# Kernel tuning notes

Hardware: AMD Instinct MI355X
Metric: run time of the kernel (lower is better)

The kernel has to match this reference:

```python
import jax, jax.numpy as jnp
import numpy as np

N_ANCHORS = 10647
N_CLASSES = 80
N_OUT = 5 + N_CLASSES
N_GT = 2048
POS_IOU = 0.7
NEG_IOU = 0.3
N_SAMPLE = 256
POS_RATIO = 0.5


def _cxcy_to_corners(b):
    return jnp.concatenate([b[:, :2] - b[:, 2:4] / 2, b[:, :2] + b[:, 2:4] / 2], axis=-1)


def _iou(a, b):
    # a: [N,4] corner boxes, b: [M,4] corner boxes -> [N,M]
    lt = jnp.maximum(a[:, None, :2], b[None, :, :2])
    rb = jnp.minimum(a[:, None, 2:], b[None, :, 2:])
    wh = jnp.clip(rb - lt, 0.0)
    inter = wh[..., 0] * wh[..., 1]
    area_a = (a[:, 2] - a[:, 0]) * (a[:, 3] - a[:, 1])
    area_b = (b[:, 2] - b[:, 0]) * (b[:, 3] - b[:, 1])
    return inter / (area_a[:, None] + area_b[None, :] - inter)


def _bce_logits(x, t):
    # numerically stable BCEWithLogits, elementwise
    return jnp.maximum(x, 0.0) - x * t + jnp.log1p(jnp.exp(-jnp.abs(x)))


def _demote_first(labels, value, excess):
    # demote the first `excess` anchors (in index order) whose label == value to -1,
    # mirroring torch's nonzero()[randperm(excess)] which always hits the first
    # `excess` entries of the nonzero list
    m = labels == value
    cum = jnp.cumsum(m.astype(jnp.int32))
    return jnp.where(m & (cum <= excess), -1.0, labels)


def _generate_targets(priors, gt_boxes, gt_labels):
    ious = _iou(_cxcy_to_corners(priors[:, :4]), _cxcy_to_corners(gt_boxes))  # [N, M]
    gt_max_index = jnp.argmax(ious, axis=0)       # [M] best anchor per gt
    anchor_max_ious = jnp.max(ious, axis=1)       # [N]
    anchor_max_index = jnp.argmax(ious, axis=1)   # [N]
    labels = jnp.full((N_ANCHORS,), -1.0, dtype=ious.dtype)
    labels = labels.at[gt_max_index].set(1.0)
    labels = jnp.where(anchor_max_ious >= POS_IOU, 1.0, labels)
    labels = jnp.where(anchor_max_ious < NEG_IOU, 0.0, labels)
    n_pos_quota = int(POS_RATIO * N_SAMPLE)
    n_pos_actual = jnp.sum(labels == 1.0)
    labels = _demote_first(labels, 1.0, jnp.maximum(n_pos_actual - n_pos_quota, 0))
    n_neg_req = N_SAMPLE - jnp.sum(labels == 1.0)
    n_neg_actual = jnp.sum(labels == 0.0)
    labels = _demote_first(labels, 0.0, jnp.maximum(n_neg_actual - n_neg_req, 0))
    anchor_gt_box = gt_boxes[anchor_max_index]    # [N,4] matched gt box per anchor
    anchor_cls = gt_labels[anchor_max_index] + 5  # [N] one-hot class column per anchor
    targets = jnp.zeros((N_ANCHORS, N_OUT), dtype=gt_boxes.dtype)
    targets = targets.at[:, :4].set(anchor_gt_box)
    targets = targets.at[:, 4].set(labels)
    targets = targets.at[jnp.arange(N_ANCHORS), anchor_cls].set(1.0)
    return targets


def _forward(predictions, gt_boxes, gt_labels, priors):
    targets = _generate_targets(priors, gt_boxes, gt_labels)
    pred = predictions[0]                          # [N, N_OUT]
    labels = targets[:, 4]
    pos = (labels == 1.0).astype(pred.dtype)
    neg = (labels == 0.0).astype(pred.dtype)
    n_pos = jnp.maximum(jnp.sum(pos), 1.0)
    n_neg = jnp.maximum(jnp.sum(neg), 1.0)
    # masked-mean MSE over x,y,w,h on positive anchors
    diff2 = (pred[:, :4] - targets[:, :4]) ** 2
    loss_box = jnp.sum(pos[:, None] * diff2, axis=0) / n_pos
    loss_conf_obj = jnp.sum(pos * _bce_logits(pred[:, 4], targets[:, 4])) / n_pos
    loss_conf_nonobj = jnp.sum(neg * _bce_logits(pred[:, 4], targets[:, 4])) / n_neg
    loss_class = jnp.sum(pos[:, None] * _bce_logits(pred[:, 5:], targets[:, 5:])) / (n_pos * N_CLASSES)
    total_loss = jnp.sum(loss_box) + loss_conf_obj + loss_conf_nonobj + loss_class
    return pred, total_loss


def setup_inputs() -> dict:
    key = jax.random.key(0)
    k1, k2, k3, k4 = jax.random.split(key, 4)
    predictions = jax.random.normal(k1, (1, N_ANCHORS, N_OUT), dtype=jnp.float32)
    gt_boxes = jax.random.uniform(k2, (N_GT, 4), dtype=jnp.float32, minval=0.05, maxval=0.95)
    gt_labels = jax.random.randint(k3, (N_GT,), 0, N_CLASSES)
    priors = jax.random.uniform(k4, (N_ANCHORS, N_OUT), dtype=jnp.float32, minval=0.05, maxval=0.95)
    return {"predictions": predictions, "gt_boxes": gt_boxes, "gt_labels": gt_labels, "priors": priors}


def reference(predictions, gt_boxes, gt_labels, priors):
    return _forward(predictions, gt_boxes, gt_labels, priors)
```

## Files before the change

kernel.cpp:

```cpp
#include <hip/hip_runtime.h>
#include <math.h>

#define N_ANCH 10647
#define N_GT   2048
#define N_OUTC 85
#define PRED_ELEMS (N_ANCH * N_OUTC)
#define PRED_V4    (PRED_ELEMS / 4)
#define N_CHUNK    42

#define ABX 21
#define ABY 32
#define NBLK_A (ABX * ABY)
#define GBX 4
#define GBY 167
#define NBLK_G (GBX * GBY)
#define NBLK_IOU (NBLK_A + NBLK_G)
#define CPY_PER_BLK ((PRED_V4 + NBLK_IOU - 1) / NBLK_IOU)

struct WS {
    unsigned long long akey[N_ANCH];
    unsigned long long gkey[N_GT];
    float acc[3];
    float pad_;
    int lab[N_ANCH];
    int cnt_p[N_CHUNK], cnt_n[N_CHUNK];
};
#define MEMSET_BYTES (N_ANCH * 8 + N_GT * 8 + 16)

__device__ __forceinline__ float bce(float x, float t) {
    return fmaxf(x, 0.0f) - x * t + log1pf(expf(-fabsf(x)));
}

__device__ __forceinline__ unsigned long long packkey(float iou, int idx) {
    return ((unsigned long long)__float_as_uint(iou) << 32) |
           (unsigned)(~(unsigned)idx);
}

__global__ __launch_bounds__(256) void k_iou(const float* __restrict__ pred,
                                             const float* __restrict__ gtb,
                                             const float* __restrict__ priors,
                                             float* __restrict__ out,
                                             WS* __restrict__ ws) {
    int b = blockIdx.x, t = threadIdx.x;
    if (t < CPY_PER_BLK) {
        int idx = b * CPY_PER_BLK + t;
        if (idx < PRED_V4)
            ((float4*)out)[idx] = ((const float4*)pred)[idx];
    }
    if (b == 0 && t == 0) {
        out[PRED_ELEMS - 3] = pred[PRED_ELEMS - 3];
        out[PRED_ELEMS - 2] = pred[PRED_ELEMS - 2];
        out[PRED_ELEMS - 1] = pred[PRED_ELEMS - 1];
    }

    __shared__ float4 sc[64];
    __shared__ float  sa[64];

    if (b < NBLK_A) {
        int bx = b % ABX, by = b / ABX;
        int jbase = by * 64;
        if (t < 64) {
            float4 v = ((const float4*)gtb)[jbase + t];
            float4 c = make_float4(v.x - v.z*0.5f, v.y - v.w*0.5f,
                                   v.x + v.z*0.5f, v.y + v.w*0.5f);
            sc[t] = c;
            sa[t] = (c.z - c.x) * (c.w - c.y);
        }
        int i0 = bx * 512 + t, i1 = i0 + 256;
        bool v0 = (i0 < N_ANCH), v1 = (i1 < N_ANCH);
        float4 a0 = make_float4(0.f,0.f,0.f,0.f), a1 = a0;
        float aa0 = 0.f, aa1 = 0.f;
        if (v0) {
            float cx = priors[i0*N_OUTC+0], cy = priors[i0*N_OUTC+1];
            float w  = priors[i0*N_OUTC+2], h  = priors[i0*N_OUTC+3];
            a0 = make_float4(cx - w*0.5f, cy - h*0.5f, cx + w*0.5f, cy + h*0.5f);
            aa0 = (a0.z - a0.x) * (a0.w - a0.y);
        }
        if (v1) {
            float cx = priors[i1*N_OUTC+0], cy = priors[i1*N_OUTC+1];
            float w  = priors[i1*N_OUTC+2], h  = priors[i1*N_OUTC+3];
            a1 = make_float4(cx - w*0.5f, cy - h*0.5f, cx + w*0.5f, cy + h*0.5f);
            aa1 = (a1.z - a1.x) * (a1.w - a1.y);
        }
        __syncthreads();
        float I0 = -1.f, S0 = 1.f, I1 = -1.f, S1 = 1.f;
        int bj0 = 0, bj1 = 0;
#pragma unroll 4
        for (int jj = 0; jj < 64; ++jj) {
            float4 g = sc[jj]; float ga = sa[jj];
            float lx = fmaxf(a0.x, g.x), ly = fmaxf(a0.y, g.y);
            float rx = fminf(a0.z, g.z), ry = fminf(a0.w, g.w);
            float In = fmaxf(rx - lx, 0.f) * fmaxf(ry - ly, 0.f);
            float Sn = aa0 + ga;
            bool c = In * S0 > I0 * Sn;
            I0 = c ? In : I0; S0 = c ? Sn : S0; bj0 = c ? jj : bj0;
            lx = fmaxf(a1.x, g.x); ly = fmaxf(a1.y, g.y);
            rx = fminf(a1.z, g.z); ry = fminf(a1.w, g.w);
            In = fmaxf(rx - lx, 0.f) * fmaxf(ry - ly, 0.f);
            Sn = aa1 + ga;
            c = In * S1 > I1 * Sn;
            I1 = c ? In : I1; S1 = c ? Sn : S1; bj1 = c ? jj : bj1;
        }
        if (v0) atomicMax(&ws->akey[i0], packkey(I0 / (S0 - I0), jbase + bj0));
        if (v1) atomicMax(&ws->akey[i1], packkey(I1 / (S1 - I1), jbase + bj1));
    } else {
        int b2 = b - NBLK_A;
        int bx = b2 % GBX, by = b2 / GBX;
        int ibase = by * 64;
        if (t < 64) {
            int i = ibase + t;
            float4 c = make_float4(0.f, 0.f, 0.f, 0.f);
            float ar = 0.f;
            if (i < N_ANCH) {
                float cx = priors[i*N_OUTC+0], cy = priors[i*N_OUTC+1];
                float w  = priors[i*N_OUTC+2], h  = priors[i*N_OUTC+3];
                c = make_float4(cx - w*0.5f, cy - h*0.5f, cx + w*0.5f, cy + h*0.5f);
                ar = (c.z - c.x) * (c.w - c.y);
            }
            sc[t] = c; sa[t] = ar;
        }
        int j0 = bx * 512 + t, j1 = j0 + 256;
        float4 v = ((const float4*)gtb)[j0];
        float4 g0 = make_float4(v.x - v.z*0.5f, v.y - v.w*0.5f,
                                v.x + v.z*0.5f, v.y + v.w*0.5f);
        float ga0 = (g0.z - g0.x) * (g0.w - g0.y);
        v = ((const float4*)gtb)[j1];
        float4 g1 = make_float4(v.x - v.z*0.5f, v.y - v.w*0.5f,
                                v.x + v.z*0.5f, v.y + v.w*0.5f);
        float ga1 = (g1.z - g1.x) * (g1.w - g1.y);
        __syncthreads();
        float I0 = -1.f, S0 = 1.f, I1 = -1.f, S1 = 1.f;
        int bi0 = 0, bi1 = 0;
#pragma unroll 4
        for (int ii = 0; ii < 64; ++ii) {
            float4 a = sc[ii]; float aa = sa[ii];
            float lx = fmaxf(a.x, g0.x), ly = fmaxf(a.y, g0.y);
            float rx = fminf(a.z, g0.z), ry = fminf(a.w, g0.w);
            float In = fmaxf(rx - lx, 0.f) * fmaxf(ry - ly, 0.f);
            float Sn = aa + ga0;
            bool c = In * S0 > I0 * Sn;
            I0 = c ? In : I0; S0 = c ? Sn : S0; bi0 = c ? ii : bi0;
            lx = fmaxf(a.x, g1.x); ly = fmaxf(a.y, g1.y);
            rx = fminf(a.z, g1.z); ry = fminf(a.w, g1.w);
            In = fmaxf(rx - lx, 0.f) * fmaxf(ry - ly, 0.f);
            Sn = aa + ga1;
            c = In * S1 > I1 * Sn;
            I1 = c ? In : I1; S1 = c ? Sn : S1; bi1 = c ? ii : bi1;
        }
        atomicMax(&ws->gkey[j0], packkey(I0 / (S0 - I0), ibase + bi0));
        atomicMax(&ws->gkey[j1], packkey(I1 / (S1 - I1), ibase + bi1));
    }
}

__global__ __launch_bounds__(256) void k_label(WS* __restrict__ ws) {
    __shared__ int flg[256];
    __shared__ int wp[4], wn[4];
    int b = blockIdx.x, t = threadIdx.x, base = b * 256;
    int lane = t & 63, wid = t >> 6;
    flg[t] = 0;
    __syncthreads();
    for (int j = t; j < N_GT; j += 256) {
        int ai = (int)(~(unsigned)(ws->gkey[j]));
        int rel = ai - base;
        if ((unsigned)rel < 256u) flg[rel] = 1;
    }
    __syncthreads();
    int i = base + t;
    int lab = -2;
    if (i < N_ANCH) {
        float amax = __uint_as_float((unsigned)(ws->akey[i] >> 32));
        lab = (amax < 0.3f) ? 0 : ((amax >= 0.7f || flg[t]) ? 1 : -1);
        ws->lab[i] = lab;
    }
    unsigned long long b1 = __ballot(lab == 1), b0 = __ballot(lab == 0);
    if (lane == 0) { wp[wid] = __popcll(b1); wn[wid] = __popcll(b0); }
    __syncthreads();
    if (t == 0) {
        ws->cnt_p[b] = wp[0] + wp[1] + wp[2] + wp[3];
        ws->cnt_n[b] = wn[0] + wn[1] + wn[2] + wn[3];
    }
}

__global__ __launch_bounds__(256) void k_closs(const float* __restrict__ pred,
                                               const float* __restrict__ gtb,
                                               const int* __restrict__ gtl,
                                               WS* __restrict__ ws) {
    __shared__ int wps[4], wns[4];
    __shared__ int    sPosI[256];
    __shared__ float4 sPosBox[256];
    __shared__ int    sPosCls[256];
    __shared__ int    sNegI[256];
    __shared__ float  red[12];
    int b = blockIdx.x, t = threadIdx.x, lane = t & 63, wid = t >> 6;

    int npa = 0, nna = 0, pb = 0, nb = 0;
#pragma unroll
    for (int c = 0; c < N_CHUNK; ++c) {
        int cp = ws->cnt_p[c], cn = ws->cnt_n[c];
        if (c < b) { pb += cp; nb += cn; }
        npa += cp; nna += cn;
    }
    int excess_pos = (npa > 128) ? (npa - 128) : 0;
    int n_pos_f = npa - excess_pos;
    int n_neg_req = 256 - n_pos_f;
    int excess_neg = (nna > n_neg_req) ? (nna - n_neg_req) : 0;

    int i = b * 256 + t;
    int lab = (i < N_ANCH) ? ws->lab[i] : -2;
    bool f1 = (lab == 1), f0 = (lab == 0);
    unsigned long long b1 = __ballot(f1), b0v = __ballot(f0);
    unsigned long long pm = (2ull << lane) - 1ull;
    int r1 = __popcll(b1 & pm), r0 = __popcll(b0v & pm);
    if (lane == 0) { wps[wid] = __popcll(b1); wns[wid] = __popcll(b0v); }
    __syncthreads();
    int p1 = 0, p0 = 0, cpB = 0, cnB = 0;
    for (int w = 0; w < 4; ++w) {
        int v1 = wps[w], v0 = wns[w];
        cpB += v1; cnB += v0;
        if (w < wid) { p1 += v1; p0 += v0; }
    }
    int thp = excess_pos - pb; thp = (thp < 0) ? 0 : thp;
    int thn = excess_neg - nb; thn = (thn < 0) ? 0 : thn;
    if (f1) {
        int L = p1 + r1;
        if (L > thp) {
            int slot = L - thp - 1;
            sPosI[slot] = i;
            unsigned am = ~(unsigned)(ws->akey[i]);
            sPosBox[slot] = ((const float4*)gtb)[am];
            sPosCls[slot] = gtl[am] + 5;
        }
    }
    if (f0) {
        int L = p0 + r0;
        if (L > thn) sNegI[L - thn - 1] = i;
    }
    __syncthreads();
    int nP = cpB - thp; nP = (nP < 0) ? 0 : nP;
    int nN = cnB - thn; nN = (nN < 0) ? 0 : nN;

    float acc_a = 0.f, acc_c = 0.f, acc_n = 0.f;
    int nT = nP * N_OUTC;
    for (int u = t; u < nT; u += 256) {
        int pi = u / N_OUTC, col = u - pi * N_OUTC;
        float p = pred[sPosI[pi] * N_OUTC + col];
        if (col < 4) {
            float d = p - ((const float*)&sPosBox[pi])[col];
            acc_a += d * d;
        } else if (col == 4) {
            acc_a += bce(p, 1.0f);
        } else {
            acc_c += bce(p, (col == sPosCls[pi]) ? 1.0f : 0.0f);
        }
    }
    for (int u = t; u < nN; u += 256)
        acc_n += bce(pred[sNegI[u] * N_OUTC + 4], 0.0f);

    for (int o = 32; o; o >>= 1) {
        acc_a += __shfl_down(acc_a, o);
        acc_c += __shfl_down(acc_c, o);
        acc_n += __shfl_down(acc_n, o);
    }
    if (lane == 0) { red[wid] = acc_a; red[4 + wid] = acc_c; red[8 + wid] = acc_n; }
    __syncthreads();
    if (t == 0) {
        float A  = red[0] + red[1] + red[2]  + red[3];
        float C  = red[4] + red[5] + red[6]  + red[7];
        float Nn = red[8] + red[9] + red[10] + red[11];
        if (A  != 0.f) atomicAdd(&ws->acc[0], A);
        if (C  != 0.f) atomicAdd(&ws->acc[1], C);
        if (Nn != 0.f) atomicAdd(&ws->acc[2], Nn);
    }
}

__global__ __launch_bounds__(64) void k_final(WS* __restrict__ ws,
                                              float* __restrict__ out) {
    int t = threadIdx.x;
    int cp = (t < N_CHUNK) ? ws->cnt_p[t] : 0;
    int cn = (t < N_CHUNK) ? ws->cnt_n[t] : 0;
    for (int o = 32; o; o >>= 1) { cp += __shfl_down(cp, o); cn += __shfl_down(cn, o); }
    if (t == 0) {
        int npa = cp, nna = cn;
        int excess_pos = (npa > 128) ? (npa - 128) : 0;
        int n_pos_f = npa - excess_pos;
        int n_neg_req = 256 - n_pos_f;
        int excess_neg = (nna > n_neg_req) ? (nna - n_neg_req) : 0;
        int n_neg_f = nna - excess_neg;
        float np = fmaxf((float)n_pos_f, 1.0f);
        float nn = fmaxf((float)n_neg_f, 1.0f);
        out[PRED_ELEMS] = ws->acc[0] / np + ws->acc[2] / nn + ws->acc[1] / (np * 80.0f);
    }
}

extern "C" void kernel_launch(void* const* d_in, const int* in_sizes, int n_in,
                              void* d_out, int out_size, void* d_ws, size_t ws_size,
                              hipStream_t stream) {
    const float* pred   = (const float*)d_in[0];
    const float* gtb    = (const float*)d_in[1];
    const int*   gtl    = (const int*)d_in[2];
    const float* priors = (const float*)d_in[3];
    float* out = (float*)d_out;
    WS* ws = (WS*)d_ws;

    hipMemsetAsync(d_ws, 0, MEMSET_BYTES, stream);
    k_iou<<<dim3(NBLK_IOU), 256, 0, stream>>>(pred, gtb, priors, out, ws);
    k_label<<<dim3(N_CHUNK), 256, 0, stream>>>(ws);
    k_closs<<<dim3(N_CHUNK), 256, 0, stream>>>(pred, gtb, gtl, ws);
    k_final<<<1, 64, 0, stream>>>(ws, out);
}
```

Measured before the change: 69.55 us.

## Fuse label, loss and final kernels into one tail kernel

Merges k_label, k_closs and k_final into a single k_tail kernel. Each block rebuilds the gt-best-anchor flags as a shared bitmap and recomputes labels and counts for all anchors redundantly, which removes the per-chunk count exchange through global memory. Each block then scales its partial losses by the final counts and atomically adds them straight into the output scalar, which k_iou zeroes first. Two kernel launches and their dependency gaps are removed, at the cost of every block scanning all anchor keys and gt keys and of float atomic accumulation order varying between runs.

```diff
diff --git a/kernel.cpp b/kernel.cpp
--- a/kernel.cpp
+++ b/kernel.cpp
@@ -7,6 +7,7 @@
 #define PRED_ELEMS (N_ANCH * N_OUTC)
 #define PRED_V4    (PRED_ELEMS / 4)
 #define N_CHUNK    42
+#define NBMW       333
 
 #define ABX 21
 #define ABY 32
@@ -20,12 +21,8 @@
 struct WS {
     unsigned long long akey[N_ANCH];
     unsigned long long gkey[N_GT];
-    float acc[3];
-    float pad_;
-    int lab[N_ANCH];
-    int cnt_p[N_CHUNK], cnt_n[N_CHUNK];
 };
-#define MEMSET_BYTES (N_ANCH * 8 + N_GT * 8 + 16)
+#define MEMSET_BYTES ((N_ANCH + N_GT) * 8)
 
 __device__ __forceinline__ float bce(float x, float t) {
     return fmaxf(x, 0.0f) - x * t + log1pf(expf(-fabsf(x)));
@@ -51,6 +48,7 @@
         out[PRED_ELEMS - 3] = pred[PRED_ELEMS - 3];
         out[PRED_ELEMS - 2] = pred[PRED_ELEMS - 2];
         out[PRED_ELEMS - 1] = pred[PRED_ELEMS - 1];
+        out[PRED_ELEMS] = 0.0f;
     }
 
     __shared__ float4 sc[64];
@@ -152,39 +150,13 @@
     }
 }
 
-__global__ __launch_bounds__(256) void k_label(WS* __restrict__ ws) {
-    __shared__ int flg[256];
-    __shared__ int wp[4], wn[4];
-    int b = blockIdx.x, t = threadIdx.x, base = b * 256;
-    int lane = t & 63, wid = t >> 6;
-    flg[t] = 0;
-    __syncthreads();
-    for (int j = t; j < N_GT; j += 256) {
-        int ai = (int)(~(unsigned)(ws->gkey[j]));
-        int rel = ai - base;
-        if ((unsigned)rel < 256u) flg[rel] = 1;
-    }
-    __syncthreads();
-    int i = base + t;
-    int lab = -2;
-    if (i < N_ANCH) {
-        float amax = __uint_as_float((unsigned)(ws->akey[i] >> 32));
-        lab = (amax < 0.3f) ? 0 : ((amax >= 0.7f || flg[t]) ? 1 : -1);
-        ws->lab[i] = lab;
-    }
-    unsigned long long b1 = __ballot(lab == 1), b0 = __ballot(lab == 0);
-    if (lane == 0) { wp[wid] = __popcll(b1); wn[wid] = __popcll(b0); }
-    __syncthreads();
-    if (t == 0) {
-        ws->cnt_p[b] = wp[0] + wp[1] + wp[2] + wp[3];
-        ws->cnt_n[b] = wn[0] + wn[1] + wn[2] + wn[3];
-    }
-}
-
-__global__ __launch_bounds__(256) void k_closs(const float* __restrict__ pred,
-                                               const float* __restrict__ gtb,
-                                               const int* __restrict__ gtl,
-                                               WS* __restrict__ ws) {
+__global__ __launch_bounds__(256) void k_tail(const float* __restrict__ pred,
+                                              const float* __restrict__ gtb,
+                                              const int* __restrict__ gtl,
+                                              WS* __restrict__ ws,
+                                              float* __restrict__ out) {
+    __shared__ unsigned fbm[NBMW];
+    __shared__ int wA[4], wB[4], wC[4], wD[4];
     __shared__ int wps[4], wns[4];
     __shared__ int    sPosI[256];
     __shared__ float4 sPosBox[256];
@@ -193,20 +165,49 @@
     __shared__ float  red[12];
     int b = blockIdx.x, t = threadIdx.x, lane = t & 63, wid = t >> 6;
 
-    int npa = 0, nna = 0, pb = 0, nb = 0;
-#pragma unroll
+    for (int k = t; k < NBMW; k += 256) fbm[k] = 0u;
+    __syncthreads();
+    for (int j = t; j < N_GT; j += 256) {
+        unsigned ai = ~(unsigned)(ws->gkey[j]);
+        atomicOr(&fbm[ai >> 5], 1u << (ai & 31));
+    }
+    __syncthreads();
+
+    const unsigned* akhi = ((const unsigned*)ws->akey) + 1;
+    int npaW = 0, nnaW = 0, pbW = 0, nbW = 0;
     for (int c = 0; c < N_CHUNK; ++c) {
-        int cp = ws->cnt_p[c], cn = ws->cnt_n[c];
-        if (c < b) { pb += cp; nb += cn; }
-        npa += cp; nna += cn;
-    }
+        int i = c * 256 + t;
+        int lab = -2;
+        if (i < N_ANCH) {
+            float amax = __uint_as_float(akhi[2 * i]);
+            bool fl = (fbm[i >> 5] >> (i & 31)) & 1u;
+            lab = (amax < 0.3f) ? 0 : ((amax >= 0.7f || fl) ? 1 : -1);
+        }
+        int c1 = __popcll(__ballot(lab == 1));
+        int c0 = __popcll(__ballot(lab == 0));
+        npaW += c1; nnaW += c0;
+        if (c < b) { pbW += c1; nbW += c0; }
+    }
+    if (lane == 0) { wA[wid] = npaW; wB[wid] = nnaW; wC[wid] = pbW; wD[wid] = nbW; }
+    __syncthreads();
+    int npa = wA[0]+wA[1]+wA[2]+wA[3];
+    int nna = wB[0]+wB[1]+wB[2]+wB[3];
+    int pb  = wC[0]+wC[1]+wC[2]+wC[3];
+    int nb  = wD[0]+wD[1]+wD[2]+wD[3];
+
     int excess_pos = (npa > 128) ? (npa - 128) : 0;
     int n_pos_f = npa - excess_pos;
     int n_neg_req = 256 - n_pos_f;
     int excess_neg = (nna > n_neg_req) ? (nna - n_neg_req) : 0;
+    int n_neg_f = nna - excess_neg;
 
     int i = b * 256 + t;
-    int lab = (i < N_ANCH) ? ws->lab[i] : -2;
+    int lab = -2;
+    if (i < N_ANCH) {
+        float amax = __uint_as_float(akhi[2 * i]);
+        bool fl = (fbm[i >> 5] >> (i & 31)) & 1u;
+        lab = (amax < 0.3f) ? 0 : ((amax >= 0.7f || fl) ? 1 : -1);
+    }
     bool f1 = (lab == 1), f0 = (lab == 0);
     unsigned long long b1 = __ballot(f1), b0v = __ballot(f0);
     unsigned long long pm = (2ull << lane) - 1ull;
@@ -267,28 +268,10 @@
         float A  = red[0] + red[1] + red[2]  + red[3];
         float C  = red[4] + red[5] + red[6]  + red[7];
         float Nn = red[8] + red[9] + red[10] + red[11];
-        if (A  != 0.f) atomicAdd(&ws->acc[0], A);
-        if (C  != 0.f) atomicAdd(&ws->acc[1], C);
-        if (Nn != 0.f) atomicAdd(&ws->acc[2], Nn);
-    }
-}
-
-__global__ __launch_bounds__(64) void k_final(WS* __restrict__ ws,
-                                              float* __restrict__ out) {
-    int t = threadIdx.x;
-    int cp = (t < N_CHUNK) ? ws->cnt_p[t] : 0;
-    int cn = (t < N_CHUNK) ? ws->cnt_n[t] : 0;
-    for (int o = 32; o; o >>= 1) { cp += __shfl_down(cp, o); cn += __shfl_down(cn, o); }
-    if (t == 0) {
-        int npa = cp, nna = cn;
-        int excess_pos = (npa > 128) ? (npa - 128) : 0;
-        int n_pos_f = npa - excess_pos;
-        int n_neg_req = 256 - n_pos_f;
-        int excess_neg = (nna > n_neg_req) ? (nna - n_neg_req) : 0;
-        int n_neg_f = nna - excess_neg;
         float np = fmaxf((float)n_pos_f, 1.0f);
         float nn = fmaxf((float)n_neg_f, 1.0f);
-        out[PRED_ELEMS] = ws->acc[0] / np + ws->acc[2] / nn + ws->acc[1] / (np * 80.0f);
+        float contrib = A / np + Nn / nn + C / (np * 80.0f);
+        if (contrib != 0.0f) atomicAdd(&out[PRED_ELEMS], contrib);
     }
 }
 
@@ -304,7 +287,5 @@
 
     hipMemsetAsync(d_ws, 0, MEMSET_BYTES, stream);
     k_iou<<<dim3(NBLK_IOU), 256, 0, stream>>>(pred, gtb, priors, out, ws);
-    k_label<<<dim3(N_CHUNK), 256, 0, stream>>>(ws);
-    k_closs<<<dim3(N_CHUNK), 256, 0, stream>>>(pred, gtb, gtl, ws);
-    k_final<<<1, 64, 0, stream>>>(ws, out);
-}
+    k_tail<<<dim3(N_CHUNK), 256, 0, stream>>>(pred, gtb, gtl, ws, out);
+}
```

After: 77.65 us. +11.7%, slower.
